# Performance work log

Measured on AMD Instinct MI355X. Metric: run time of the kernel, lower is better.

The kernel has to match this reference:

```python
import jax, jax.numpy as jnp
import numpy as np

B, S, D, E, K = 4, 4096, 2048, 64, 2
LN_EPS = 1e-5
TEMP_EPS = 1e-6
Z_LOSS_COEF = 0.001
LB_COEF = 0.1


def setup_inputs() -> dict:
    key = jax.random.key(0)
    k1, k2 = jax.random.split(key)
    x = jax.random.normal(k1, (B, S, D), dtype=jnp.float32)
    # kaiming_normal fan_in (std = 1/sqrt(D)) scaled by 0.01, as in __init__
    W = jax.random.normal(k2, (E, D), dtype=jnp.float32) * jnp.float32(0.01 / np.sqrt(D))
    gamma = jnp.ones((E,), jnp.float32)   # LayerNorm weight
    beta = jnp.zeros((E,), jnp.float32)   # LayerNorm bias
    temperature = jnp.full((1,), 0.5, jnp.float32)
    return {"x": x, "W": W, "gamma": gamma, "beta": beta, "temperature": temperature}


def reference(x, W, gamma, beta, temperature):
    b, s, d = x.shape
    xf = x.reshape(-1, d)                                  # [N, D]
    logits = xf @ W.T                                      # [N, E]
    # LayerNorm over expert dim (biased variance, eps=1e-5, matches torch)
    mu = logits.mean(axis=-1, keepdims=True)
    var = jnp.mean(jnp.square(logits - mu), axis=-1, keepdims=True)
    logits = (logits - mu) * jax.lax.rsqrt(var + LN_EPS) * gamma + beta
    # temperature-scaled softmax
    routing_weights = jax.nn.softmax(logits / (temperature + TEMP_EPS), axis=-1)  # [N, E]
    # top-k + scatter into dense dispatch mask
    top_w, top_idx = jax.lax.top_k(routing_weights, K)     # [N, K]
    n = routing_weights.shape[0]
    dispatch = jnp.zeros_like(routing_weights).at[jnp.arange(n)[:, None], top_idx].set(top_w)
    dispatch = dispatch.reshape(b, s, E)                   # [B, S, E]
    # aux losses
    expert_load = dispatch.mean(axis=1)                    # [B, E]
    load_balance_loss = jnp.std(expert_load, ddof=1) / expert_load.mean() * 10.0
    router_z_loss = jnp.mean(jnp.square(logits))
    total_loss = ZLC * router_z_loss + LB_COEF * load_balance_loss if False else (
        Z_LOSS_COEF * router_z_loss + LB_COEF * load_balance_loss)
    return jax.lax.stop_gradient(routing_weights), dispatch, total_loss
```

## Files before the change

kernel.cpp:

```cpp
#include <hip/hip_runtime.h>
#include <hip/hip_bf16.h>
#include <float.h>
#include <math.h>

#define B_DIM 4
#define S_DIM 4096
#define D_DIM 2048
#define E_DIM 64
#define N_TOK 16384
#define TOKS 32
#define NBLK (N_TOK / TOKS)
#define NTHR 512
#define BK 64
#define LDK 72
#define SLICES 4
#define DSLICE (D_DIM / SLICES)
#define KSTEPS (DSLICE / BK)
#define GAP_THRESH 1e-3f
#define MAXFLAG 16

typedef __bf16 bf16x8_t __attribute__((ext_vector_type(8)));
typedef float f32x4_t __attribute__((ext_vector_type(4)));

union U8 { bf16x8_t v; unsigned short u[8]; };

__device__ __forceinline__ void split2(float f, unsigned short& h, unsigned short& l) {
    unsigned int u = __float_as_uint(f);
    h = (unsigned short)(u >> 16);
    float hf = __uint_as_float(u & 0xFFFF0000u);
    l = (unsigned short)(__float_as_uint(f - hf) >> 16);
}

__global__ __launch_bounds__(NTHR, 4) void router_main(
    const float* __restrict__ x, const float* __restrict__ W,
    const float* __restrict__ gamma, const float* __restrict__ beta,
    const float* __restrict__ temperature,
    float* __restrict__ out_rw, float* __restrict__ out_dp,
    float* __restrict__ g_zsum, float* __restrict__ g_load)
{
    __shared__ __align__(16) unsigned char shraw[SLICES * 64 * LDK * 2 * 2];
    typedef unsigned short WPlane[64][LDK];
    WPlane* const wh = (WPlane*)shraw;
    WPlane* const wl = (WPlane*)(shraw + SLICES * 64 * LDK * sizeof(unsigned short));
    typedef float PartT[TOKS][E_DIM + 2];
    PartT* const part = (PartT*)shraw;
    float (* const lgt)[E_DIM + 1] =
        (float (*)[E_DIM + 1])(shraw + SLICES * TOKS * (E_DIM + 2) * sizeof(float));

    __shared__ float lgm[E_DIM], lbt[E_DIM], loadsum[E_DIM];
    __shared__ float smu[TOKS], srs[TOKS], sinv[TOKS];
    __shared__ int sel1[TOKS], sel2[TOKS];
    __shared__ int ftok[MAXFLAG], fcand[MAXFLAG][3];
    __shared__ int nflag;

    const int tid = threadIdx.x;
    const int tokBase = blockIdx.x * TOKS;
    const int lane = tid & 63;
    const int wv = tid >> 6;
    const int g  = wv & 1;
    const int sl = wv >> 1;
    const int l15 = lane & 15;
    const int quad = lane >> 4;

    if (tid == 0) nflag = 0;
    if (tid < E_DIM) { lgm[tid] = gamma[tid]; lbt[tid] = beta[tid]; loadsum[tid] = 0.f; }

    const int sslice = tid >> 7;
    const int rowW = (tid & 127) >> 1;
    const int colW = (tid & 1) * 32;
    const float* wp = W + (size_t)rowW * D_DIM + sslice * DSLICE + colW;

    const float* xp = x + (size_t)(tokBase + g * 16 + l15) * D_DIM + sl * DSLICE + quad * 8;

    f32x4_t acc[4];
    #pragma unroll
    for (int t = 0; t < 4; ++t) acc[t] = (f32x4_t){0.f, 0.f, 0.f, 0.f};

    float4 wreg[8], xq[4], xn[4];
    #pragma unroll
    for (int j = 0; j < 8; ++j) wreg[j] = *(const float4*)(wp + j * 4);
    #pragma unroll
    for (int c = 0; c < 2; ++c) {
        xq[c * 2]     = *(const float4*)(xp + c * 32);
        xq[c * 2 + 1] = *(const float4*)(xp + c * 32 + 4);
    }
    #pragma unroll
    for (int j = 0; j < 8; ++j) {
        ushort4 h, l;
        split2(wreg[j].x, h.x, l.x); split2(wreg[j].y, h.y, l.y);
        split2(wreg[j].z, h.z, l.z); split2(wreg[j].w, h.w, l.w);
        *(ushort4*)&wh[sslice][rowW][colW + j * 4] = h;
        *(ushort4*)&wl[sslice][rowW][colW + j * 4] = l;
    }
    __syncthreads();

    for (int s = 0; s < KSTEPS; ++s) {
        const bool more = (s + 1 < KSTEPS);
        if (more) {
            const float* wq = wp + (s + 1) * BK;
            #pragma unroll
            for (int j = 0; j < 8; ++j) wreg[j] = *(const float4*)(wq + j * 4);
            const float* xg = xp + (s + 1) * BK;
            #pragma unroll
            for (int c = 0; c < 2; ++c) {
                xn[c * 2]     = *(const float4*)(xg + c * 32);
                xn[c * 2 + 1] = *(const float4*)(xg + c * 32 + 4);
            }
        }
        #pragma unroll
        for (int h = 0; h < 2; ++h) {
            float tf[8] = {xq[h*2].x, xq[h*2].y, xq[h*2].z, xq[h*2].w,
                           xq[h*2+1].x, xq[h*2+1].y, xq[h*2+1].z, xq[h*2+1].w};
            U8 ah, al;
            #pragma unroll
            for (int k = 0; k < 8; ++k) split2(tf[k], ah.u[k], al.u[k]);
            #pragma unroll
            for (int t = 0; t < 4; ++t) {
                U8 bh, bl;
                bh.v = *(const bf16x8_t*)&wh[sl][t * 16 + l15][h * 32 + quad * 8];
                bl.v = *(const bf16x8_t*)&wl[sl][t * 16 + l15][h * 32 + quad * 8];
                acc[t] = __builtin_amdgcn_mfma_f32_16x16x32_bf16(ah.v, bh.v, acc[t], 0, 0, 0);
                acc[t] = __builtin_amdgcn_mfma_f32_16x16x32_bf16(ah.v, bl.v, acc[t], 0, 0, 0);
                acc[t] = __builtin_amdgcn_mfma_f32_16x16x32_bf16(al.v, bh.v, acc[t], 0, 0, 0);
            }
        }
        __syncthreads();
        if (more) {
            #pragma unroll
            for (int j = 0; j < 8; ++j) {
                ushort4 h, l;
                split2(wreg[j].x, h.x, l.x); split2(wreg[j].y, h.y, l.y);
                split2(wreg[j].z, h.z, l.z); split2(wreg[j].w, h.w, l.w);
                *(ushort4*)&wh[sslice][rowW][colW + j * 4] = h;
                *(ushort4*)&wl[sslice][rowW][colW + j * 4] = l;
            }
            #pragma unroll
            for (int j = 0; j < 4; ++j) xq[j] = xn[j];
            __syncthreads();
        }
    }

    #pragma unroll
    for (int t = 0; t < 4; ++t)
        #pragma unroll
        for (int r = 0; r < 4; ++r)
            part[sl][g * 16 + quad * 4 + r][t * 16 + l15] = acc[t][r];
    __syncthreads();

    for (int i = tid; i < TOKS * E_DIM; i += NTHR) {
        int r = i >> 6, c = i & 63;
        lgt[r][c] = (part[0][r][c] + part[1][r][c]) + (part[2][r][c] + part[3][r][c]);
    }
    __syncthreads();

    if (wv < 2) {
        const int tok = wv * 16 + l15;
        const int q = quad;
        const float it = 1.f / (temperature[0] + 1e-6f);
        float s1 = 0.f, s2 = 0.f;
        #pragma unroll
        for (int e = 0; e < 16; ++e) { float v = lgt[tok][q * 16 + e]; s1 += v; s2 += v * v; }
        s1 += __shfl_xor(s1, 16); s1 += __shfl_xor(s1, 32);
        s2 += __shfl_xor(s2, 16); s2 += __shfl_xor(s2, 32);
        const float mu  = s1 * (1.f / 64.f);
        const float var = s2 * (1.f / 64.f) - mu * mu;
        const float rs  = rsqrtf(var + 1e-5f);
        if (q == 0) { smu[tok] = mu; srs[tok] = rs; }

        float m0 = -FLT_MAX, m1 = -FLT_MAX, m2 = -FLT_MAX;
        int   i0 = -1, i1 = -1, i2 = -1;
        float zl = 0.f;
        #pragma unroll
        for (int e = 0; e < 16; ++e) {
            int c = q * 16 + e;
            float y = (lgt[tok][c] - mu) * rs * lgm[c] + lbt[c];
            lgt[tok][c] = y;
            zl += y * y;
            if (y > m0)      { m2 = m1; i2 = i1; m1 = m0; i1 = i0; m0 = y; i0 = c; }
            else if (y > m1) { m2 = m1; i2 = i1; m1 = y; i1 = c; }
            else if (y > m2) { m2 = y; i2 = c; }
        }
        #pragma unroll
        for (int d = 16; d <= 32; d <<= 1) {
            float n0 = __shfl_xor(m0, d), n1 = __shfl_xor(m1, d), n2 = __shfl_xor(m2, d);
            int   j0 = __shfl_xor(i0, d), j1 = __shfl_xor(i1, d), j2 = __shfl_xor(i2, d);
            bool t0 = (m0 > n0) || (m0 == n0 && i0 < j0);
            float r0v = t0 ? m0 : n0; int r0i = t0 ? i0 : j0;
            float A0v = t0 ? m1 : m0; int A0i = t0 ? i1 : i0;
            float A1v = t0 ? m2 : m1; int A1i = t0 ? i2 : i1;
            float B0v = t0 ? n0 : n1; int B0i = t0 ? j0 : j1;
            float B1v = t0 ? n1 : n2; int B1i = t0 ? j1 : j2;
            bool t1 = (A0v > B0v) || (A0v == B0v && A0i < B0i);
            float r1v = t1 ? A0v : B0v; int r1i = t1 ? A0i : B0i;
            float A0w = t1 ? A1v : A0v; int A0j = t1 ? A1i : A0i;
            float B0w = t1 ? B0v : B1v; int B0j = t1 ? B0i : B1i;
            bool t2 = (A0w > B0w) || (A0w == B0w && A0j < B0j);
            float r2v = t2 ? A0w : B0w; int r2i = t2 ? A0j : B0j;
            m0 = r0v; i0 = r0i; m1 = r1v; i1 = r1i; m2 = r2v; i2 = r2i;
        }
        if (q == 0) {
            sel1[tok] = i0; sel2[tok] = i1;
            if (m1 - m2 < GAP_THRESH) {
                int sf = atomicAdd(&nflag, 1);
                if (sf < MAXFLAG) { ftok[sf] = tok; fcand[sf][0] = i0; fcand[sf][1] = i1; fcand[sf][2] = i2; }
            }
        }
        float es = 0.f;
        #pragma unroll
        for (int e = 0; e < 16; ++e) {
            int c = q * 16 + e;
            float ev = __expf((lgt[tok][c] - m0) * it);
            lgt[tok][c] = ev; es += ev;
        }
        es += __shfl_xor(es, 16); es += __shfl_xor(es, 32);
        if (q == 0) sinv[tok] = 1.f / es;
        zl += __shfl_xor(zl, 1); zl += __shfl_xor(zl, 2); zl += __shfl_xor(zl, 4);
        zl += __shfl_xor(zl, 8); zl += __shfl_xor(zl, 16); zl += __shfl_xor(zl, 32);
        if (lane == 0) atomicAdd(g_zsum, zl);
    }
    __syncthreads();

    const int nf = min(nflag, MAXFLAG);
    for (int f = wv; f < nf; f += 8) {
        const int tk = ftok[f];
        const int c0 = fcand[f][0], c1 = fcand[f][1], c2 = fcand[f][2];
        const float* xr = x + (size_t)(tokBase + tk) * D_DIM;
        const float* w0 = W + (size_t)c0 * D_DIM;
        const float* w1 = W + (size_t)c1 * D_DIM;
        const float* w2 = W + (size_t)c2 * D_DIM;
        double L0 = 0.0, L1 = 0.0, L2 = 0.0;
        for (int i = lane; i < D_DIM; i += 64) {
            double xv = (double)xr[i];
            L0 += xv * (double)w0[i];
            L1 += xv * (double)w1[i];
            L2 += xv * (double)w2[i];
        }
        #pragma unroll
        for (int off = 32; off; off >>= 1) {
            L0 += __shfl_down(L0, off);
            L1 += __shfl_down(L1, off);
            L2 += __shfl_down(L2, off);
        }
        if (lane == 0) {
            double dmu = (double)smu[tk], drs = (double)srs[tk];
            double y0 = (L0 - dmu) * drs * (double)lgm[c0] + (double)lbt[c0];
            double y1 = (L1 - dmu) * drs * (double)lgm[c1] + (double)lbt[c1];
            double y2 = (L2 - dmu) * drs * (double)lgm[c2] + (double)lbt[c2];
            bool g01 = (y0 > y1) || (y0 == y1 && c0 < c1);
            bool g02 = (y0 > y2) || (y0 == y2 && c0 < c2);
            bool g12 = (y1 > y2) || (y1 == y2 && c1 < c2);
            int a, b;
            if (!g01 && !g02)      { a = c1; b = c2; }
            else if (g01 && !g12)  { a = c0; b = c2; }
            else                   { a = c0; b = c1; }
            sel1[tk] = a; sel2[tk] = b;
        }
    }
    __syncthreads();

    if (tid < TOKS) {
        float inv = sinv[tid];
        atomicAdd(&loadsum[sel1[tid]], lgt[tid][sel1[tid]] * inv);
        atomicAdd(&loadsum[sel2[tid]], lgt[tid][sel2[tid]] * inv);
    }
    __syncthreads();
    if (tid < E_DIM) atomicAdd(&g_load[(tokBase >> 12) * E_DIM + tid], loadsum[tid]);

    float* orw = out_rw + (size_t)tokBase * E_DIM;
    float* odp = out_dp + (size_t)tokBase * E_DIM;
    for (int i = tid; i < TOKS * E_DIM; i += NTHR) {
        int r = i >> 6, c = i & 63;
        float p = lgt[r][c] * sinv[r];
        orw[i] = p;
        odp[i] = (c == sel1[r] || c == sel2[r]) ? p : 0.f;
    }
}

__global__ void router_fin(const float* __restrict__ ws, float* __restrict__ out_loss) {
    __shared__ float sv[B_DIM * E_DIM];
    const int tid = threadIdx.x;
    sv[tid] = ws[8 + tid] * (1.f / S_DIM);
    __syncthreads();
    if (tid == 0) {
        float s = 0.f;
        for (int i = 0; i < B_DIM * E_DIM; ++i) s += sv[i];
        const float mean = s * (1.f / (B_DIM * E_DIM));
        float ss = 0.f;
        for (int i = 0; i < B_DIM * E_DIM; ++i) { float d = sv[i] - mean; ss += d * d; }
        const float sd = sqrtf(ss * (1.f / (B_DIM * E_DIM - 1)));
        const float z = ws[0] * (1.f / ((float)N_TOK * E_DIM));
        out_loss[0] = 0.001f * z + 0.1f * (sd / mean) * 10.f;
    }
}

extern "C" void kernel_launch(void* const* d_in, const int* in_sizes, int n_in,
                              void* d_out, int out_size, void* d_ws, size_t ws_size,
                              hipStream_t stream) {
    const float* x     = (const float*)d_in[0];
    const float* W     = (const float*)d_in[1];
    const float* gamma = (const float*)d_in[2];
    const float* beta  = (const float*)d_in[3];
    const float* temp  = (const float*)d_in[4];
    float* out  = (float*)d_out;
    float* rw   = out;
    float* dp   = out + (size_t)N_TOK * E_DIM;
    float* loss = out + 2 * (size_t)N_TOK * E_DIM;
    float* ws   = (float*)d_ws;

    hipMemsetAsync(d_ws, 0, 512 * sizeof(float), stream);
    router_main<<<dim3(NBLK), dim3(NTHR), 0, stream>>>(x, W, gamma, beta, temp,
                                                       rw, dp, ws, ws + 8);
    router_fin<<<dim3(1), dim3(256), 0, stream>>>(ws, loss);
}
```

Baseline: 236.1 us.

## Pre-split W into bf16 hi/lo planes once and read from global

Adds a small pre-kernel that splits W into bf16 high and low planes in workspace and also zeroes the loss accumulators, which replaces the memset. The main kernel then loads the B fragments directly from global memory (cache-resident, 512KB) instead of each block re-splitting W and staging it through LDS with two barriers per K-step. This removes the redundant per-block conversion work and the synchronisation. In exchange, every wave reads W fragments straight from L2 with no sharing across waves, and the main kernel has less latency hiding because the loads are no longer prefetched.

```diff
diff --git a/kernel.cpp b/kernel.cpp
--- a/kernel.cpp
+++ b/kernel.cpp
@@ -12,7 +12,6 @@
 #define NBLK (N_TOK / TOKS)
 #define NTHR 512
 #define BK 64
-#define LDK 72
 #define SLICES 4
 #define DSLICE (D_DIM / SLICES)
 #define KSTEPS (DSLICE / BK)
@@ -31,22 +30,28 @@
     l = (unsigned short)(__float_as_uint(f - hf) >> 16);
 }
 
+__global__ void wsplit(const float* __restrict__ W, unsigned short* __restrict__ wh,
+                       unsigned short* __restrict__ wl, float* __restrict__ wshdr) {
+    const int i = blockIdx.x * 256 + threadIdx.x;
+    if (blockIdx.x == 0) { wshdr[threadIdx.x] = 0.f; wshdr[threadIdx.x + 256] = 0.f; }
+    float4 v = *(const float4*)(W + (size_t)i * 4);
+    ushort4 h, l;
+    split2(v.x, h.x, l.x); split2(v.y, h.y, l.y);
+    split2(v.z, h.z, l.z); split2(v.w, h.w, l.w);
+    *(ushort4*)(wh + (size_t)i * 4) = h;
+    *(ushort4*)(wl + (size_t)i * 4) = l;
+}
+
 __global__ __launch_bounds__(NTHR, 4) void router_main(
     const float* __restrict__ x, const float* __restrict__ W,
+    const unsigned short* __restrict__ whg, const unsigned short* __restrict__ wlg,
     const float* __restrict__ gamma, const float* __restrict__ beta,
     const float* __restrict__ temperature,
     float* __restrict__ out_rw, float* __restrict__ out_dp,
     float* __restrict__ g_zsum, float* __restrict__ g_load)
 {
-    __shared__ __align__(16) unsigned char shraw[SLICES * 64 * LDK * 2 * 2];
-    typedef unsigned short WPlane[64][LDK];
-    WPlane* const wh = (WPlane*)shraw;
-    WPlane* const wl = (WPlane*)(shraw + SLICES * 64 * LDK * sizeof(unsigned short));
-    typedef float PartT[TOKS][E_DIM + 2];
-    PartT* const part = (PartT*)shraw;
-    float (* const lgt)[E_DIM + 1] =
-        (float (*)[E_DIM + 1])(shraw + SLICES * TOKS * (E_DIM + 2) * sizeof(float));
-
+    __shared__ float part[SLICES][TOKS][E_DIM + 2];
+    __shared__ float lgt[TOKS][E_DIM + 1];
     __shared__ float lgm[E_DIM], lbt[E_DIM], loadsum[E_DIM];
     __shared__ float smu[TOKS], srs[TOKS], sinv[TOKS];
     __shared__ int sel1[TOKS], sel2[TOKS];
@@ -65,41 +70,32 @@
     if (tid == 0) nflag = 0;
     if (tid < E_DIM) { lgm[tid] = gamma[tid]; lbt[tid] = beta[tid]; loadsum[tid] = 0.f; }
 
-    const int sslice = tid >> 7;
-    const int rowW = (tid & 127) >> 1;
-    const int colW = (tid & 1) * 32;
-    const float* wp = W + (size_t)rowW * D_DIM + sslice * DSLICE + colW;
-
     const float* xp = x + (size_t)(tokBase + g * 16 + l15) * D_DIM + sl * DSLICE + quad * 8;
+
+    const unsigned short* wb[4][2];
+    {
+        const size_t lanepos = (size_t)l15 * D_DIM + sl * DSLICE + quad * 8;
+        #pragma unroll
+        for (int t = 0; t < 4; ++t) {
+            wb[t][0] = whg + lanepos + (size_t)t * 16 * D_DIM;
+            wb[t][1] = wlg + lanepos + (size_t)t * 16 * D_DIM;
+        }
+    }
 
     f32x4_t acc[4];
     #pragma unroll
     for (int t = 0; t < 4; ++t) acc[t] = (f32x4_t){0.f, 0.f, 0.f, 0.f};
 
-    float4 wreg[8], xq[4], xn[4];
-    #pragma unroll
-    for (int j = 0; j < 8; ++j) wreg[j] = *(const float4*)(wp + j * 4);
+    float4 xq[4], xn[4];
     #pragma unroll
     for (int c = 0; c < 2; ++c) {
         xq[c * 2]     = *(const float4*)(xp + c * 32);
         xq[c * 2 + 1] = *(const float4*)(xp + c * 32 + 4);
     }
-    #pragma unroll
-    for (int j = 0; j < 8; ++j) {
-        ushort4 h, l;
-        split2(wreg[j].x, h.x, l.x); split2(wreg[j].y, h.y, l.y);
-        split2(wreg[j].z, h.z, l.z); split2(wreg[j].w, h.w, l.w);
-        *(ushort4*)&wh[sslice][rowW][colW + j * 4] = h;
-        *(ushort4*)&wl[sslice][rowW][colW + j * 4] = l;
-    }
-    __syncthreads();
 
     for (int s = 0; s < KSTEPS; ++s) {
         const bool more = (s + 1 < KSTEPS);
         if (more) {
-            const float* wq = wp + (s + 1) * BK;
-            #pragma unroll
-            for (int j = 0; j < 8; ++j) wreg[j] = *(const float4*)(wq + j * 4);
             const float* xg = xp + (s + 1) * BK;
             #pragma unroll
             for (int c = 0; c < 2; ++c) {
@@ -109,6 +105,12 @@
         }
         #pragma unroll
         for (int h = 0; h < 2; ++h) {
+            bf16x8_t bh[4], bl[4];
+            #pragma unroll
+            for (int t = 0; t < 4; ++t) {
+                bh[t] = *(const bf16x8_t*)(wb[t][0] + s * BK + h * 32);
+                bl[t] = *(const bf16x8_t*)(wb[t][1] + s * BK + h * 32);
+            }
             float tf[8] = {xq[h*2].x, xq[h*2].y, xq[h*2].z, xq[h*2].w,
                            xq[h*2+1].x, xq[h*2+1].y, xq[h*2+1].z, xq[h*2+1].w};
             U8 ah, al;
@@ -116,27 +118,14 @@
             for (int k = 0; k < 8; ++k) split2(tf[k], ah.u[k], al.u[k]);
             #pragma unroll
             for (int t = 0; t < 4; ++t) {
-                U8 bh, bl;
-                bh.v = *(const bf16x8_t*)&wh[sl][t * 16 + l15][h * 32 + quad * 8];
-                bl.v = *(const bf16x8_t*)&wl[sl][t * 16 + l15][h * 32 + quad * 8];
-                acc[t] = __builtin_amdgcn_mfma_f32_16x16x32_bf16(ah.v, bh.v, acc[t], 0, 0, 0);
-                acc[t] = __builtin_amdgcn_mfma_f32_16x16x32_bf16(ah.v, bl.v, acc[t], 0, 0, 0);
-                acc[t] = __builtin_amdgcn_mfma_f32_16x16x32_bf16(al.v, bh.v, acc[t], 0, 0, 0);
+                acc[t] = __builtin_amdgcn_mfma_f32_16x16x32_bf16(ah.v, bh[t], acc[t], 0, 0, 0);
+                acc[t] = __builtin_amdgcn_mfma_f32_16x16x32_bf16(ah.v, bl[t], acc[t], 0, 0, 0);
+                acc[t] = __builtin_amdgcn_mfma_f32_16x16x32_bf16(al.v, bh[t], acc[t], 0, 0, 0);
             }
         }
-        __syncthreads();
         if (more) {
             #pragma unroll
-            for (int j = 0; j < 8; ++j) {
-                ushort4 h, l;
-                split2(wreg[j].x, h.x, l.x); split2(wreg[j].y, h.y, l.y);
-                split2(wreg[j].z, h.z, l.z); split2(wreg[j].w, h.w, l.w);
-                *(ushort4*)&wh[sslice][rowW][colW + j * 4] = h;
-                *(ushort4*)&wl[sslice][rowW][colW + j * 4] = l;
-            }
-            #pragma unroll
             for (int j = 0; j < 4; ++j) xq[j] = xn[j];
-            __syncthreads();
         }
     }
 
@@ -307,8 +296,11 @@
     float* loss = out + 2 * (size_t)N_TOK * E_DIM;
     float* ws   = (float*)d_ws;
 
-    hipMemsetAsync(d_ws, 0, 512 * sizeof(float), stream);
-    router_main<<<dim3(NBLK), dim3(NTHR), 0, stream>>>(x, W, gamma, beta, temp,
+    unsigned short* whg = (unsigned short*)((char*)d_ws + 4096);
+    unsigned short* wlg = whg + (size_t)E_DIM * D_DIM;
+
+    wsplit<<<dim3(128), dim3(256), 0, stream>>>(W, whg, wlg, ws);
+    router_main<<<dim3(NBLK), dim3(NTHR), 0, stream>>>(x, W, whg, wlg, gamma, beta, temp,
                                                        rw, dp, ws, ws + 8);
     router_fin<<<dim3(1), dim3(256), 0, stream>>>(ws, loss);
 }
```

Result: slower. 261.6 us (+10.8%).
